# Kernel tuning notes

Hardware: AMD Instinct MI355X
Metric: run time of the kernel (lower is better)

## Reference

```python
import jax, jax.numpy as jnp
import numpy as np

N = 1_000_000   # gaussians
K_NB = 10       # neighbor control points per gaussian
K_TOTAL = 300   # num_fine control points


def _normalize(q, eps=1e-8):
    return q / jnp.maximum(jnp.linalg.norm(q, axis=-1, keepdims=True), eps)


def quaternion_to_rotation_matrix(q):
    # q: [..., 4] in (w, x, y, z); normalized before conversion
    q = _normalize(q)
    w, x, y, z = q[..., 0], q[..., 1], q[..., 2], q[..., 3]
    R = jnp.stack([
        jnp.stack([1 - 2 * (y * y + z * z), 2 * (x * y - w * z), 2 * (x * z + w * y)], axis=-1),
        jnp.stack([2 * (x * y + w * z), 1 - 2 * (x * x + z * z), 2 * (y * z - w * x)], axis=-1),
        jnp.stack([2 * (x * z - w * y), 2 * (y * z + w * x), 1 - 2 * (x * x + y * y)], axis=-1),
    ], axis=-2)  # [..., 3, 3]
    return R


def quaternion_multiply(a, b):
    # Hamilton product, (w, x, y, z)
    aw, ax, ay, az = a[..., 0], a[..., 1], a[..., 2], a[..., 3]
    bw, bx, by, bz = b[..., 0], b[..., 1], b[..., 2], b[..., 3]
    return jnp.stack([
        aw * bw - ax * bx - ay * by - az * bz,
        aw * bx + ax * bw + ay * bz - az * by,
        aw * by - ax * bz + ay * bw + az * bx,
        aw * bz + ax * by - ay * bx + az * bw,
    ], axis=-1)


def setup_inputs() -> dict:
    key = jax.random.key(0)
    ks = jax.random.split(key, 7)
    means = jax.random.normal(ks[0], (N, 3), dtype=jnp.float32)
    quaternions = _normalize(jax.random.normal(ks[1], (N, 4), dtype=jnp.float32))
    w = jax.random.uniform(ks[2], (N, K_NB), dtype=jnp.float32) + 1e-3
    weights = w / w.sum(-1, keepdims=True)  # blending weights sum to 1
    indices = jax.random.randint(ks[3], (N, K_NB), 0, K_TOTAL)
    ctrl_translations = 0.1 * jax.random.normal(ks[4], (K_TOTAL, 3), dtype=jnp.float32)
    ctrl_rotations = _normalize(jax.random.normal(ks[5], (K_TOTAL, 4), dtype=jnp.float32))
    ctrl_positions = jax.random.normal(ks[6], (K_TOTAL, 3), dtype=jnp.float32)
    return {
        'means': means, 'quaternions': quaternions, 'weights': weights,
        'ctrl_translations': ctrl_translations, 'ctrl_rotations': ctrl_rotations,
        'ctrl_positions': ctrl_positions, 'indices': indices,
    }


def reference(means, quaternions, weights, ctrl_translations, ctrl_rotations, ctrl_positions, indices):
    # gather neighbor control-point transforms
    nb_trans = ctrl_translations[indices]   # [N, K, 3]
    nb_rots = ctrl_rotations[indices]       # [N, K, 4]
    nb_pos = ctrl_positions[indices]        # [N, K, 3]

    diff = means[:, None, :] - nb_pos                       # [N, K, 3]
    R_ctrl = quaternion_to_rotation_matrix(nb_rots)         # [N, K, 3, 3]
    rotated_diff = jnp.einsum('nkij,nkj->nki', R_ctrl, diff)
    deformed_per_cp = rotated_diff + nb_pos + nb_trans      # [N, K, 3]

    w = weights[..., None]                                  # [N, K, 1]
    deformed_means = (w * deformed_per_cp).sum(axis=1)      # [N, 3]

    blended_rot = _normalize((w * nb_rots).sum(axis=1))     # [N, 4]
    deformed_quats = quaternion_multiply(blended_rot, quaternions)
    return deformed_means, deformed_quats
```

## Files before the change

### kernel.cpp

```cpp
#include <hip/hip_runtime.h>
#include <math.h>


template <int KNB>
__global__ __launch_bounds__(512, 6) void deform_kernel(
    const float* __restrict__ means,
    const float* __restrict__ quats,
    const float* __restrict__ weights,
    const float* __restrict__ ctrl_trans,
    const float* __restrict__ ctrl_rot,
    const float* __restrict__ ctrl_pos,
    const int*   __restrict__ indices,
    float* __restrict__ out_means,
    float* __restrict__ out_quats,
    int N, int K_TOTAL)
{
    extern __shared__ float4 s4[];

    const int i = blockIdx.x * blockDim.x + threadIdx.x;
    const bool active = i < N;

    int   idx[KNB];
    float wt[KNB];
    float mx = 0.f, my = 0.f, mz = 0.f;
    float4 g = make_float4(0.f, 0.f, 0.f, 0.f);
    if (active) {
        const int*   idx_row = indices + (long long)i * KNB;
        const float* w_row   = weights + (long long)i * KNB;
        const int2*   ip = (const int2*)idx_row;
        const float2* wp = (const float2*)w_row;
#pragma unroll
        for (int k = 0; k < KNB / 2; k++) {
            int2 iv = ip[k];
            float2 wv = wp[k];
            idx[2 * k] = iv.x; idx[2 * k + 1] = iv.y;
            wt[2 * k] = wv.x;  wt[2 * k + 1] = wv.y;
        }
        if (KNB & 1) { idx[KNB - 1] = idx_row[KNB - 1]; wt[KNB - 1] = w_row[KNB - 1]; }
        mx = means[i * 3 + 0];
        my = means[i * 3 + 1];
        mz = means[i * 3 + 2];
        g = ((const float4*)quats)[i];
    }

    for (int cp = threadIdx.x; cp < K_TOTAL; cp += blockDim.x) {
        float qw = ctrl_rot[cp * 4 + 0];
        float qx = ctrl_rot[cp * 4 + 1];
        float qy = ctrl_rot[cp * 4 + 2];
        float qz = ctrl_rot[cp * 4 + 3];
        float n  = sqrtf(qw * qw + qx * qx + qy * qy + qz * qz);
        float inv = 1.0f / fmaxf(n, 1e-8f);
        float w = qw * inv, x = qx * inv, y = qy * inv, z = qz * inv;
        float R00 = 1.0f - 2.0f * (y * y + z * z);
        float R01 = 2.0f * (x * y - w * z);
        float R02 = 2.0f * (x * z + w * y);
        float R10 = 2.0f * (x * y + w * z);
        float R11 = 1.0f - 2.0f * (x * x + z * z);
        float R12 = 2.0f * (y * z - w * x);
        float R20 = 2.0f * (x * z - w * y);
        float R21 = 2.0f * (y * z + w * x);
        float R22 = 1.0f - 2.0f * (x * x + y * y);
        float px = ctrl_pos[cp * 3 + 0];
        float py = ctrl_pos[cp * 3 + 1];
        float pz = ctrl_pos[cp * 3 + 2];
        float tx = ctrl_trans[cp * 3 + 0];
        float ty = ctrl_trans[cp * 3 + 1];
        float tz = ctrl_trans[cp * 3 + 2];
        float bx = px + tx - (R00 * px + R01 * py + R02 * pz);
        float by = py + ty - (R10 * px + R11 * py + R12 * pz);
        float bz = pz + tz - (R20 * px + R21 * py + R22 * pz);
        s4[cp * 5 + 0] = make_float4(R00, R01, R02, R10);
        s4[cp * 5 + 1] = make_float4(R11, R12, R20, R21);
        s4[cp * 5 + 2] = make_float4(R22, bx, by, bz);
        s4[cp * 5 + 3] = make_float4(qw, qx, qy, qz);
    }
    __syncthreads();

    if (!active) return;

    float dmx = 0.f, dmy = 0.f, dmz = 0.f;
    float qaw = 0.f, qax = 0.f, qay = 0.f, qaz = 0.f;

#pragma unroll
    for (int k = 0; k < KNB; k++) {
        int   cp = idx[k];
        float w  = wt[k];
        float4 a = s4[cp * 5 + 0];
        float4 b = s4[cp * 5 + 1];
        float4 c = s4[cp * 5 + 2];
        float4 d = s4[cp * 5 + 3];
        float rx = fmaf(a.x, mx, fmaf(a.y, my, fmaf(a.z, mz, c.y)));
        float ry = fmaf(a.w, mx, fmaf(b.x, my, fmaf(b.y, mz, c.z)));
        float rz = fmaf(b.z, mx, fmaf(b.w, my, fmaf(c.x, mz, c.w)));
        dmx = fmaf(w, rx, dmx);
        dmy = fmaf(w, ry, dmy);
        dmz = fmaf(w, rz, dmz);
        qaw = fmaf(w, d.x, qaw);
        qax = fmaf(w, d.y, qax);
        qay = fmaf(w, d.z, qay);
        qaz = fmaf(w, d.w, qaz);
    }

    out_means[i * 3 + 0] = dmx;
    out_means[i * 3 + 1] = dmy;
    out_means[i * 3 + 2] = dmz;

    float n   = sqrtf(qaw * qaw + qax * qax + qay * qay + qaz * qaz);
    float inv = 1.0f / fmaxf(n, 1e-8f);
    float bw = qaw * inv, bx = qax * inv, by = qay * inv, bz = qaz * inv;

    float gw = g.x, gx = g.y, gy = g.z, gz = g.w;
    float ow = bw * gw - bx * gx - by * gy - bz * gz;
    float ox = bw * gx + bx * gw + by * gz - bz * gy;
    float oy = bw * gy - bx * gz + by * gw + bz * gx;
    float oz = bw * gz + bx * gy - by * gx + bz * gw;

    ((float4*)(out_quats))[i] = make_float4(ow, ox, oy, oz);
}

extern "C" void kernel_launch(void* const* d_in, const int* in_sizes, int n_in,
                              void* d_out, int out_size, void* d_ws, size_t ws_size,
                              hipStream_t stream) {
    const float* means      = (const float*)d_in[0];
    const float* quats      = (const float*)d_in[1];
    const float* weights    = (const float*)d_in[2];
    const float* ctrl_trans = (const float*)d_in[3];
    const float* ctrl_rot   = (const float*)d_in[4];
    const float* ctrl_pos   = (const float*)d_in[5];
    const int*   indices    = (const int*)d_in[6];

    int N       = in_sizes[0] / 3;
    int K_NB    = in_sizes[2] / N;
    int K_TOTAL = in_sizes[3] / 3;

    float* out_means = (float*)d_out;
    float* out_quats = (float*)d_out + (long long)N * 3;

    int block = 512;
    int grid  = (N + block - 1) / block;
    size_t smem = (size_t)K_TOTAL * 5 * sizeof(float4);

    if (K_NB == 10) {
        deform_kernel<10><<<grid, block, smem, stream>>>(
            means, quats, weights, ctrl_trans, ctrl_rot, ctrl_pos, indices,
            out_means, out_quats, N, K_TOTAL);
    } else if (K_NB == 8) {
        deform_kernel<8><<<grid, block, smem, stream>>>(
            means, quats, weights, ctrl_trans, ctrl_rot, ctrl_pos, indices,
            out_means, out_quats, N, K_TOTAL);
    } else if (K_NB == 16) {
        deform_kernel<16><<<grid, block, smem, stream>>>(
            means, quats, weights, ctrl_trans, ctrl_rot, ctrl_pos, indices,
            out_means, out_quats, N, K_TOTAL);
    } else {
        deform_kernel<10><<<grid, block, smem, stream>>>(
            means, quats, weights, ctrl_trans, ctrl_rot, ctrl_pos, indices,
            out_means, out_quats, N, K_TOTAL);
    }
}
```

Baseline: 149.5 us.

## Use persistent grid-stride loop with prefetch and compact quaternion LDS table

Replaces the one-thread-per-gaussian launch with a fixed 512-block persistent grid. Each thread loops over gaussians and prefetches the next one's indices, weights, mean and quaternion while computing the current one. The per-control-point LDS table shrinks from five float4 (rotation matrix) to two (normalized quaternion plus norm and offset), and means are rotated with a cross-product quaternion formula. This cuts LDS traffic and setup work per block, and the prefetch is meant to hide global load latency. In exchange it adds ALU work per neighbor and register pressure, and launch bounds drop to 4 waves.

```diff
diff --git a/kernel.cpp b/kernel.cpp
--- a/kernel.cpp
+++ b/kernel.cpp
@@ -2,8 +2,20 @@
 #include <math.h>
 
 
+__device__ __forceinline__ float3 quat_rotate(float qw, float qx, float qy, float qz,
+                                              float vx, float vy, float vz) {
+    float cx = qy * vz - qz * vy;
+    float cy = qz * vx - qx * vz;
+    float cz = qx * vy - qy * vx;
+    float tx = cx + cx, ty = cy + cy, tz = cz + cz;
+    float rx = fmaf(qy, tz, fmaf(-qz, ty, fmaf(qw, tx, vx)));
+    float ry = fmaf(qz, tx, fmaf(-qx, tz, fmaf(qw, ty, vy)));
+    float rz = fmaf(qx, ty, fmaf(-qy, tx, fmaf(qw, tz, vz)));
+    return make_float3(rx, ry, rz);
+}
+
 template <int KNB>
-__global__ __launch_bounds__(512, 6) void deform_kernel(
+__global__ __launch_bounds__(512, 4) void deform_kernel(
     const float* __restrict__ means,
     const float* __restrict__ quats,
     const float* __restrict__ weights,
@@ -15,107 +27,165 @@
     float* __restrict__ out_quats,
     int N, int K_TOTAL)
 {
-    extern __shared__ float4 s4[];
-
-    const int i = blockIdx.x * blockDim.x + threadIdx.x;
-    const bool active = i < N;
+    extern __shared__ float4 sT[];
+
+    const long long gstride = (long long)gridDim.x * blockDim.x;
+    long long i = (long long)blockIdx.x * blockDim.x + threadIdx.x;
+    bool act = i < N;
 
     int   idx[KNB];
     float wt[KNB];
     float mx = 0.f, my = 0.f, mz = 0.f;
     float4 g = make_float4(0.f, 0.f, 0.f, 0.f);
-    if (active) {
-        const int*   idx_row = indices + (long long)i * KNB;
-        const float* w_row   = weights + (long long)i * KNB;
-        const int2*   ip = (const int2*)idx_row;
-        const float2* wp = (const float2*)w_row;
+    if (act) {
+        const int2*   ip = (const int2*)(indices + i * KNB);
+        const float2* wp = (const float2*)(weights + i * KNB);
 #pragma unroll
         for (int k = 0; k < KNB / 2; k++) {
-            int2 iv = ip[k];
-            float2 wv = wp[k];
+            int2 iv = ip[k]; float2 wv = wp[k];
             idx[2 * k] = iv.x; idx[2 * k + 1] = iv.y;
             wt[2 * k] = wv.x;  wt[2 * k + 1] = wv.y;
         }
-        if (KNB & 1) { idx[KNB - 1] = idx_row[KNB - 1]; wt[KNB - 1] = w_row[KNB - 1]; }
-        mx = means[i * 3 + 0];
-        my = means[i * 3 + 1];
-        mz = means[i * 3 + 2];
+        if (KNB & 1) { idx[KNB-1] = indices[i*KNB + KNB-1]; wt[KNB-1] = weights[i*KNB + KNB-1]; }
+        mx = means[i * 3 + 0]; my = means[i * 3 + 1]; mz = means[i * 3 + 2];
         g = ((const float4*)quats)[i];
     }
 
     for (int cp = threadIdx.x; cp < K_TOTAL; cp += blockDim.x) {
-        float qw = ctrl_rot[cp * 4 + 0];
-        float qx = ctrl_rot[cp * 4 + 1];
-        float qy = ctrl_rot[cp * 4 + 2];
-        float qz = ctrl_rot[cp * 4 + 3];
-        float n  = sqrtf(qw * qw + qx * qx + qy * qy + qz * qz);
+        float4 q = ((const float4*)ctrl_rot)[cp];
+        float n   = sqrtf(q.x*q.x + q.y*q.y + q.z*q.z + q.w*q.w);
         float inv = 1.0f / fmaxf(n, 1e-8f);
-        float w = qw * inv, x = qx * inv, y = qy * inv, z = qz * inv;
-        float R00 = 1.0f - 2.0f * (y * y + z * z);
-        float R01 = 2.0f * (x * y - w * z);
-        float R02 = 2.0f * (x * z + w * y);
-        float R10 = 2.0f * (x * y + w * z);
-        float R11 = 1.0f - 2.0f * (x * x + z * z);
-        float R12 = 2.0f * (y * z - w * x);
-        float R20 = 2.0f * (x * z - w * y);
-        float R21 = 2.0f * (y * z + w * x);
-        float R22 = 1.0f - 2.0f * (x * x + y * y);
-        float px = ctrl_pos[cp * 3 + 0];
-        float py = ctrl_pos[cp * 3 + 1];
-        float pz = ctrl_pos[cp * 3 + 2];
-        float tx = ctrl_trans[cp * 3 + 0];
-        float ty = ctrl_trans[cp * 3 + 1];
-        float tz = ctrl_trans[cp * 3 + 2];
-        float bx = px + tx - (R00 * px + R01 * py + R02 * pz);
-        float by = py + ty - (R10 * px + R11 * py + R12 * pz);
-        float bz = pz + tz - (R20 * px + R21 * py + R22 * pz);
-        s4[cp * 5 + 0] = make_float4(R00, R01, R02, R10);
-        s4[cp * 5 + 1] = make_float4(R11, R12, R20, R21);
-        s4[cp * 5 + 2] = make_float4(R22, bx, by, bz);
-        s4[cp * 5 + 3] = make_float4(qw, qx, qy, qz);
+        float qw = q.x*inv, qx = q.y*inv, qy = q.z*inv, qz = q.w*inv;
+        float px = ctrl_pos[cp*3+0], py = ctrl_pos[cp*3+1], pz = ctrl_pos[cp*3+2];
+        float tx = ctrl_trans[cp*3+0], ty = ctrl_trans[cp*3+1], tz = ctrl_trans[cp*3+2];
+        float3 rp = quat_rotate(qw, qx, qy, qz, px, py, pz);
+        float bx = px + tx - rp.x;
+        float by = py + ty - rp.y;
+        float bz = pz + tz - rp.z;
+        sT[cp * 3 + 0] = make_float4(qw, qx, qy, qz);
+        sT[cp * 3 + 1] = make_float4(n, bx, by, bz);
     }
     __syncthreads();
 
-    if (!active) return;
-
+    while (act) {
+        long long inext = i + gstride;
+        bool actn = inext < N;
+
+        int   idx2[KNB];
+        float wt2[KNB];
+        float mx2 = 0.f, my2 = 0.f, mz2 = 0.f;
+        float4 g2 = make_float4(0.f, 0.f, 0.f, 0.f);
+        if (actn) {
+            const int2*   ip = (const int2*)(indices + inext * KNB);
+            const float2* wp = (const float2*)(weights + inext * KNB);
+#pragma unroll
+            for (int k = 0; k < KNB / 2; k++) {
+                int2 iv = ip[k]; float2 wv = wp[k];
+                idx2[2 * k] = iv.x; idx2[2 * k + 1] = iv.y;
+                wt2[2 * k] = wv.x;  wt2[2 * k + 1] = wv.y;
+            }
+            if (KNB & 1) { idx2[KNB-1] = indices[inext*KNB + KNB-1]; wt2[KNB-1] = weights[inext*KNB + KNB-1]; }
+            mx2 = means[inext * 3 + 0]; my2 = means[inext * 3 + 1]; mz2 = means[inext * 3 + 2];
+            g2 = ((const float4*)quats)[inext];
+        }
+
+        float dmx = 0.f, dmy = 0.f, dmz = 0.f;
+        float qaw = 0.f, qax = 0.f, qay = 0.f, qaz = 0.f;
+
+#pragma unroll
+        for (int k = 0; k < KNB; k++) {
+            int   cp = idx[k];
+            float w  = wt[k];
+            float4 qh = sT[cp * 3 + 0];
+            float4 nb = sT[cp * 3 + 1];
+            float3 r  = quat_rotate(qh.x, qh.y, qh.z, qh.w, mx, my, mz);
+            dmx = fmaf(w, r.x + nb.y, dmx);
+            dmy = fmaf(w, r.y + nb.z, dmy);
+            dmz = fmaf(w, r.z + nb.w, dmz);
+            float wn = w * nb.x;
+            qaw = fmaf(wn, qh.x, qaw);
+            qax = fmaf(wn, qh.y, qax);
+            qay = fmaf(wn, qh.z, qay);
+            qaz = fmaf(wn, qh.w, qaz);
+        }
+
+        out_means[i * 3 + 0] = dmx;
+        out_means[i * 3 + 1] = dmy;
+        out_means[i * 3 + 2] = dmz;
+
+        float n   = sqrtf(qaw*qaw + qax*qax + qay*qay + qaz*qaz);
+        float inv = 1.0f / fmaxf(n, 1e-8f);
+        float bw = qaw*inv, bx = qax*inv, by = qay*inv, bz = qaz*inv;
+        float gw = g.x, gx = g.y, gy = g.z, gz = g.w;
+        float ow = bw*gw - bx*gx - by*gy - bz*gz;
+        float ox = bw*gx + bx*gw + by*gz - bz*gy;
+        float oy = bw*gy - bx*gz + by*gw + bz*gx;
+        float oz = bw*gz + bx*gy - by*gx + bz*gw;
+        ((float4*)out_quats)[i] = make_float4(ow, ox, oy, oz);
+
+#pragma unroll
+        for (int k = 0; k < KNB; k++) { idx[k] = idx2[k]; wt[k] = wt2[k]; }
+        mx = mx2; my = my2; mz = mz2; g = g2;
+        i = inext; act = actn;
+    }
+}
+
+__global__ __launch_bounds__(512, 4) void deform_kernel_generic(
+    const float* __restrict__ means,
+    const float* __restrict__ quats,
+    const float* __restrict__ weights,
+    const float* __restrict__ ctrl_trans,
+    const float* __restrict__ ctrl_rot,
+    const float* __restrict__ ctrl_pos,
+    const int*   __restrict__ indices,
+    float* __restrict__ out_means,
+    float* __restrict__ out_quats,
+    int N, int K_NB, int K_TOTAL)
+{
+    extern __shared__ float4 sT[];
+    for (int cp = threadIdx.x; cp < K_TOTAL; cp += blockDim.x) {
+        float4 q = ((const float4*)ctrl_rot)[cp];
+        float n   = sqrtf(q.x*q.x + q.y*q.y + q.z*q.z + q.w*q.w);
+        float inv = 1.0f / fmaxf(n, 1e-8f);
+        float qw = q.x*inv, qx = q.y*inv, qy = q.z*inv, qz = q.w*inv;
+        float px = ctrl_pos[cp*3+0], py = ctrl_pos[cp*3+1], pz = ctrl_pos[cp*3+2];
+        float tx = ctrl_trans[cp*3+0], ty = ctrl_trans[cp*3+1], tz = ctrl_trans[cp*3+2];
+        float3 rp = quat_rotate(qw, qx, qy, qz, px, py, pz);
+        sT[cp * 3 + 0] = make_float4(qw, qx, qy, qz);
+        sT[cp * 3 + 1] = make_float4(n, px + tx - rp.x, py + ty - rp.y, pz + tz - rp.z);
+    }
+    __syncthreads();
+
+    long long i = (long long)blockIdx.x * blockDim.x + threadIdx.x;
+    if (i >= N) return;
+
+    float mx = means[i*3+0], my = means[i*3+1], mz = means[i*3+2];
     float dmx = 0.f, dmy = 0.f, dmz = 0.f;
     float qaw = 0.f, qax = 0.f, qay = 0.f, qaz = 0.f;
-
-#pragma unroll
-    for (int k = 0; k < KNB; k++) {
-        int   cp = idx[k];
-        float w  = wt[k];
-        float4 a = s4[cp * 5 + 0];
-        float4 b = s4[cp * 5 + 1];
-        float4 c = s4[cp * 5 + 2];
-        float4 d = s4[cp * 5 + 3];
-        float rx = fmaf(a.x, mx, fmaf(a.y, my, fmaf(a.z, mz, c.y)));
-        float ry = fmaf(a.w, mx, fmaf(b.x, my, fmaf(b.y, mz, c.z)));
-        float rz = fmaf(b.z, mx, fmaf(b.w, my, fmaf(c.x, mz, c.w)));
-        dmx = fmaf(w, rx, dmx);
-        dmy = fmaf(w, ry, dmy);
-        dmz = fmaf(w, rz, dmz);
-        qaw = fmaf(w, d.x, qaw);
-        qax = fmaf(w, d.y, qax);
-        qay = fmaf(w, d.z, qay);
-        qaz = fmaf(w, d.w, qaz);
-    }
-
-    out_means[i * 3 + 0] = dmx;
-    out_means[i * 3 + 1] = dmy;
-    out_means[i * 3 + 2] = dmz;
-
-    float n   = sqrtf(qaw * qaw + qax * qax + qay * qay + qaz * qaz);
+    for (int k = 0; k < K_NB; k++) {
+        int   cp = indices[i * K_NB + k];
+        float w  = weights[i * K_NB + k];
+        float4 qh = sT[cp * 3 + 0];
+        float4 nb = sT[cp * 3 + 1];
+        float3 r  = quat_rotate(qh.x, qh.y, qh.z, qh.w, mx, my, mz);
+        dmx = fmaf(w, r.x + nb.y, dmx);
+        dmy = fmaf(w, r.y + nb.z, dmy);
+        dmz = fmaf(w, r.z + nb.w, dmz);
+        float wn = w * nb.x;
+        qaw = fmaf(wn, qh.x, qaw); qax = fmaf(wn, qh.y, qax);
+        qay = fmaf(wn, qh.z, qay); qaz = fmaf(wn, qh.w, qaz);
+    }
+    out_means[i*3+0] = dmx; out_means[i*3+1] = dmy; out_means[i*3+2] = dmz;
+    float n   = sqrtf(qaw*qaw + qax*qax + qay*qay + qaz*qaz);
     float inv = 1.0f / fmaxf(n, 1e-8f);
-    float bw = qaw * inv, bx = qax * inv, by = qay * inv, bz = qaz * inv;
-
-    float gw = g.x, gx = g.y, gy = g.z, gz = g.w;
-    float ow = bw * gw - bx * gx - by * gy - bz * gz;
-    float ox = bw * gx + bx * gw + by * gz - bz * gy;
-    float oy = bw * gy - bx * gz + by * gw + bz * gx;
-    float oz = bw * gz + bx * gy - by * gx + bz * gw;
-
-    ((float4*)(out_quats))[i] = make_float4(ow, ox, oy, oz);
+    float bw = qaw*inv, bx = qax*inv, by = qay*inv, bz = qaz*inv;
+    float4 gq = ((const float4*)quats)[i];
+    float gw = gq.x, gx = gq.y, gy = gq.z, gz = gq.w;
+    ((float4*)out_quats)[i] = make_float4(
+        bw*gw - bx*gx - by*gy - bz*gz,
+        bw*gx + bx*gw + by*gz - bz*gy,
+        bw*gy - bx*gz + by*gw + bz*gx,
+        bw*gz + bx*gy - by*gx + bz*gw);
 }
 
 extern "C" void kernel_launch(void* const* d_in, const int* in_sizes, int n_in,
@@ -136,25 +206,25 @@
     float* out_means = (float*)d_out;
     float* out_quats = (float*)d_out + (long long)N * 3;
 
-    int block = 512;
-    int grid  = (N + block - 1) / block;
-    size_t smem = (size_t)K_TOTAL * 5 * sizeof(float4);
-
-    if (K_NB == 10) {
-        deform_kernel<10><<<grid, block, smem, stream>>>(
+    const int block = 512;
+    size_t smem = (size_t)K_TOTAL * 3 * sizeof(float4);
+
+    if (K_NB == 10 || K_NB == 8 || K_NB == 16 || K_NB == 4 || K_NB == 6 || K_NB == 12) {
+        int grid = 512;
+        int needed = (int)((N + (long long)block - 1) / block);
+        if (needed < grid) grid = needed;
+        switch (K_NB) {
+        case 4:  deform_kernel<4 ><<<grid, block, smem, stream>>>(means, quats, weights, ctrl_trans, ctrl_rot, ctrl_pos, indices, out_means, out_quats, N, K_TOTAL); break;
+        case 6:  deform_kernel<6 ><<<grid, block, smem, stream>>>(means, quats, weights, ctrl_trans, ctrl_rot, ctrl_pos, indices, out_means, out_quats, N, K_TOTAL); break;
+        case 8:  deform_kernel<8 ><<<grid, block, smem, stream>>>(means, quats, weights, ctrl_trans, ctrl_rot, ctrl_pos, indices, out_means, out_quats, N, K_TOTAL); break;
+        case 10: deform_kernel<10><<<grid, block, smem, stream>>>(means, quats, weights, ctrl_trans, ctrl_rot, ctrl_pos, indices, out_means, out_quats, N, K_TOTAL); break;
+        case 12: deform_kernel<12><<<grid, block, smem, stream>>>(means, quats, weights, ctrl_trans, ctrl_rot, ctrl_pos, indices, out_means, out_quats, N, K_TOTAL); break;
+        case 16: deform_kernel<16><<<grid, block, smem, stream>>>(means, quats, weights, ctrl_trans, ctrl_rot, ctrl_pos, indices, out_means, out_quats, N, K_TOTAL); break;
+        }
+    } else {
+        int grid = (int)((N + (long long)block - 1) / block);
+        deform_kernel_generic<<<grid, block, smem, stream>>>(
             means, quats, weights, ctrl_trans, ctrl_rot, ctrl_pos, indices,
-            out_means, out_quats, N, K_TOTAL);
-    } else if (K_NB == 8) {
-        deform_kernel<8><<<grid, block, smem, stream>>>(
-            means, quats, weights, ctrl_trans, ctrl_rot, ctrl_pos, indices,
-            out_means, out_quats, N, K_TOTAL);
-    } else if (K_NB == 16) {
-        deform_kernel<16><<<grid, block, smem, stream>>>(
-            means, quats, weights, ctrl_trans, ctrl_rot, ctrl_pos, indices,
-            out_means, out_quats, N, K_TOTAL);
-    } else {
-        deform_kernel<10><<<grid, block, smem, stream>>>(
-            means, quats, weights, ctrl_trans, ctrl_rot, ctrl_pos, indices,
-            out_means, out_quats, N, K_TOTAL);
-    }
-}
+            out_means, out_quats, N, K_NB, K_TOTAL);
+    }
+}
```

Result: slower. 231.7 us (+55.0%).
